# Kernel tuning notes

Hardware: AMD Instinct MI355X
Metric: run time of the kernel (lower is better)

Reference implementation:

```python
import jax, jax.numpy as jnp
import numpy as np

HID = 64
EPS = 1e-12  # tf.contrib.layers.layer_norm variance_epsilon


def _ln(x, g, b):
    m = jnp.mean(x, axis=-1, keepdims=True)
    v = jnp.mean(jnp.square(x - m), axis=-1, keepdims=True)
    return (x - m) * jax.lax.rsqrt(v + EPS) * g + b


def setup_inputs() -> dict:
    key = jax.random.key(0)
    k1, k2, k3, k4 = jax.random.split(key, 4)
    N, T, OBS, ACT = 2048, 256, 96, 32
    D = OBS + ACT
    obss = jax.random.normal(k1, (N, T, OBS), dtype=jnp.float32)
    actions = jax.random.normal(k2, (N, T, ACT), dtype=jnp.float32)
    W = jax.random.normal(k3, (D + HID, 4 * HID), dtype=jnp.float32) * (1.0 / np.sqrt(D + HID))
    ln_gamma = jnp.ones((5, HID), dtype=jnp.float32)   # i, j, f, o, state norms
    ln_beta = jnp.zeros((5, HID), dtype=jnp.float32)
    dense_W = jax.random.uniform(k4, (HID, 1), dtype=jnp.float32, minval=-0.003, maxval=0.003)
    dense_b = jnp.zeros((1,), dtype=jnp.float32)
    return {"obss": obss, "actions": actions, "W": W, "ln_gamma": ln_gamma,
            "ln_beta": ln_beta, "dense_W": dense_W, "dense_b": dense_b}


def reference(obss, actions, W, ln_gamma, ln_beta, dense_W, dense_b):
    # [N,T,obs+act] -> time-major [T,N,D]
    x = jnp.concatenate([obss, actions], axis=-1)
    xt = jnp.transpose(x, (1, 0, 2))
    N = x.shape[0]
    c0 = jnp.zeros((N, HID), dtype=x.dtype)
    h0 = jnp.zeros((N, HID), dtype=x.dtype)
    forget_bias = jnp.asarray(1.0, dtype=x.dtype)

    def step(carry, x_t):
        c, h = carry
        z = jnp.concatenate([x_t, h], axis=-1) @ W  # [N, 4*HID], no bias
        i, j, f, o = jnp.split(z, 4, axis=-1)
        i = _ln(i, ln_gamma[0], ln_beta[0])
        j = _ln(j, ln_gamma[1], ln_beta[1])
        f = _ln(f, ln_gamma[2], ln_beta[2])
        o = _ln(o, ln_gamma[3], ln_beta[3])
        new_c = c * jax.nn.sigmoid(f + forget_bias) + jax.nn.sigmoid(i) * jnp.tanh(j)
        new_c = _ln(new_c, ln_gamma[4], ln_beta[4])
        new_h = jnp.tanh(new_c) * jax.nn.sigmoid(o)
        return (new_c, new_h), new_h

    _, hs = jax.lax.scan(step, (c0, h0), xt)  # hs: [T,N,HID]
    outputs = jnp.transpose(hs, (1, 0, 2))     # [N,T,HID]
    q = outputs @ dense_W + dense_b            # [N,T,1]
    return q
```

## Files before the change

### kernel.cpp

```cpp
#include <hip/hip_runtime.h>

#define TT 256
#define OBS 96
#define ACTD 32
#define RPB 8
#define CH 8
#define XCS 136
#define ZXS 12
#define ZBS 69
#define HBS 80
#define EPS 1e-12f

typedef _Float16 f16x8 __attribute__((ext_vector_type(8)));
typedef float f32x4 __attribute__((ext_vector_type(4)));
typedef unsigned short u16x8 __attribute__((ext_vector_type(8)));
typedef unsigned int u32;
typedef unsigned short u16;

__device__ __forceinline__ u16 f2h(float f) {
  return __builtin_bit_cast(u16, (_Float16)f);
}
__device__ __forceinline__ u32 pk2h(float a, float b) {
  return (u32)f2h(a) | ((u32)f2h(b) << 16);
}
__device__ __forceinline__ float sigm(float x) { return 1.0f / (1.0f + __expf(-x)); }
__device__ __forceinline__ float tanh_(float x) { return 1.0f - 2.0f / (__expf(2.0f * x) + 1.0f); }

template <int CTRL>
__device__ __forceinline__ float dpp_add(float x) {
  int t = __builtin_amdgcn_update_dpp(0, __builtin_bit_cast(int, x), CTRL, 0xF, 0xF, true);
  return x + __builtin_bit_cast(float, t);
}
__device__ __forceinline__ float red16(float x) {
  x = dpp_add<0xB1>(x);
  x = dpp_add<0x4E>(x);
  x = dpp_add<0x124>(x);
  x = dpp_add<0x128>(x);
  return x;
}
__device__ __forceinline__ float red64(float x) {
  x = red16(x);
  x += __shfl_xor(x, 16, 64);
  x += __shfl_xor(x, 32, 64);
  return x;
}

__device__ __forceinline__ void barrier_lds() {
  __builtin_amdgcn_sched_barrier(0);
  asm volatile("s_waitcnt lgkmcnt(0)" ::: "memory");
  __builtin_amdgcn_s_barrier();
  __builtin_amdgcn_sched_barrier(0);
}

__global__ __launch_bounds__(512, 2) void lstm_fused(
    const float* __restrict__ obss, const float* __restrict__ actions,
    const float* __restrict__ Wm, const float* __restrict__ gamma,
    const float* __restrict__ beta, const float* __restrict__ dWv,
    const float* __restrict__ dbv, float* __restrict__ out)
{
  __shared__ u16 xchunk[CH][RPB][XCS];
  __shared__ float zxT[CH][256][ZXS];
  __shared__ float zbuf[4][16][ZBS];
  __shared__ float pbuf[4][16][4];
  __shared__ u16 hh[CH][RPB][HBS];

  const int tid = threadIdx.x;
  const int wv = tid >> 6;
  const int ln = tid & 63;
  const int l15 = ln & 15;
  const int quad = ln >> 4;
  const int g = wv & 3;
  const int half = wv >> 2;
  const int n0 = blockIdx.x * RPB;
  const int c0 = g * 64 + half * 32 + l15;

  for (int i = tid; i < CH * RPB * HBS / 2; i += 512) ((u32*)hh)[i] = 0u;

  u16x8 bw[6][2];
  #pragma unroll
  for (int kt = 0; kt < 6; ++kt)
    #pragma unroll
    for (int nt = 0; nt < 2; ++nt)
      #pragma unroll
      for (int j = 0; j < 8; ++j)
        bw[kt][nt][j] = f2h(Wm[(kt * 32 + quad * 8 + j) * 256 + c0 + nt * 16]);

  float ggam[4], gbet[4];
  #pragma unroll
  for (int gg = 0; gg < 4; ++gg) {
    ggam[gg] = gamma[gg * 64 + ln];
    gbet[gg] = beta[gg * 64 + ln];
  }
  const float cgam = gamma[4 * 64 + ln], cbet = beta[4 * 64 + ln];
  const float dw = dWv[ln];
  const float bias = dbv[0];

  const int sp = tid >> 8;
  const int srow = (tid >> 5) & 7;
  const int slot = tid & 31;
  const float* obs_p = obss + (size_t)(n0 + srow) * TT * OBS;
  const float* act_p = actions + (size_t)(n0 + srow) * TT * ACTD;

  f32x4 xst[4];
  #pragma unroll
  for (int k = 0; k < 4; ++k) {
    const int s = sp + 2 * k;
    xst[k] = (slot < 24) ? *(const f32x4*)(obs_p + s * OBS + slot * 4)
                         : *(const f32x4*)(act_p + s * ACTD + (slot - 24) * 4);
  }
  #pragma unroll
  for (int k = 0; k < 4; ++k) {
    const int s = sp + 2 * k;
    *(uint2*)&xchunk[s][srow][slot * 4] =
        make_uint2(pk2h(xst[k][0], xst[k][1]), pk2h(xst[k][2], xst[k][3]));
  }

  float creg = 0.0f;
  f32x4 zs0p, zs1p;
  __syncthreads();

  for (int t = 0; t < TT; ++t) {
    const int tm = t & 7;
    const int tp = (t + 7) & 7;

    if (tm == 0) {
      if (t > 0) {
        #pragma unroll
        for (int s = 0; s < CH; ++s) {
          const float hv = (float)__builtin_bit_cast(_Float16, hh[s][wv][ln]);
          const float qv = red64(hv * dw);
          if (ln == 0) out[(size_t)(n0 + wv) * TT + (t - 8) + s] = qv + bias;
        }
      }
      #pragma unroll
      for (int k = 0; k < 4; ++k) {
        int tl = t + 8 + sp + 2 * k; if (tl > TT - 1) tl = TT - 1;
        xst[k] = (slot < 24) ? *(const f32x4*)(obs_p + tl * OBS + slot * 4)
                             : *(const f32x4*)(act_p + tl * ACTD + (slot - 24) * 4);
      }
      #pragma unroll
      for (int s = 0; s < CH; ++s) {
        u16x8 afx[4];
        #pragma unroll
        for (int kt = 0; kt < 4; ++kt)
          afx[kt] = *(const u16x8*)&xchunk[s][l15 & 7][kt * 32 + quad * 8];
        f32x4 ax0 = {0.f, 0.f, 0.f, 0.f}, ax1 = ax0;
        #pragma unroll
        for (int kt = 0; kt < 4; ++kt) {
          ax0 = __builtin_amdgcn_mfma_f32_16x16x32_f16(
              __builtin_bit_cast(f16x8, afx[kt]), __builtin_bit_cast(f16x8, bw[kt][0]), ax0, 0, 0, 0);
          ax1 = __builtin_amdgcn_mfma_f32_16x16x32_f16(
              __builtin_bit_cast(f16x8, afx[kt]), __builtin_bit_cast(f16x8, bw[kt][1]), ax1, 0, 0, 0);
        }
        if (quad < 2) {
          *(f32x4*)&zxT[s][c0][quad * 4] = ax0;
          *(f32x4*)&zxT[s][c0 + 16][quad * 4] = ax1;
        }
      }
    }

    const u16x8 afh0 = *(const u16x8*)&hh[tp][l15 & 7][quad * 8];
    const u16x8 afh1 = *(const u16x8*)&hh[tp][l15 & 7][32 + quad * 8];
    const f32x4 zs0 = (tm == 0) ? *(const f32x4*)&zxT[0][c0][(quad & 1) * 4] : zs0p;
    const f32x4 zs1 = (tm == 0) ? *(const f32x4*)&zxT[0][c0 + 16][(quad & 1) * 4] : zs1p;
    f32x4 acc0 = __builtin_amdgcn_mfma_f32_16x16x32_f16(
        __builtin_bit_cast(f16x8, afh0), __builtin_bit_cast(f16x8, bw[4][0]), zs0, 0, 0, 0);
    f32x4 acc1 = __builtin_amdgcn_mfma_f32_16x16x32_f16(
        __builtin_bit_cast(f16x8, afh0), __builtin_bit_cast(f16x8, bw[4][1]), zs1, 0, 0, 0);
    acc0 = __builtin_amdgcn_mfma_f32_16x16x32_f16(
        __builtin_bit_cast(f16x8, afh1), __builtin_bit_cast(f16x8, bw[5][0]), acc0, 0, 0, 0);
    acc1 = __builtin_amdgcn_mfma_f32_16x16x32_f16(
        __builtin_bit_cast(f16x8, afh1), __builtin_bit_cast(f16x8, bw[5][1]), acc1, 0, 0, 0);

    #pragma unroll
    for (int r = 0; r < 4; ++r) {
      zbuf[g][quad * 4 + r][half * 32 + l15]      = acc0[r];
      zbuf[g][quad * 4 + r][half * 32 + 16 + l15] = acc1[r];
    }
    float s[4], ss[4];
    #pragma unroll
    for (int r = 0; r < 4; ++r) {
      s[r]  = red16(acc0[r] + acc1[r]);
      ss[r] = red16(acc0[r] * acc0[r] + acc1[r] * acc1[r]);
    }
    if (l15 < 4) {
      const float sv  = l15 == 0 ? s[0]  : l15 == 1 ? s[1]  : l15 == 2 ? s[2]  : s[3];
      const float ssv = l15 == 0 ? ss[0] : l15 == 1 ? ss[1] : l15 == 2 ? ss[2] : ss[3];
      *(float2*)&pbuf[g][quad * 4 + l15][half * 2] = make_float2(sv, ssv);
    }
    barrier_lds();

    if (tm != 7) {
      zs0p = *(const f32x4*)&zxT[tm + 1][c0][(quad & 1) * 4];
      zs1p = *(const f32x4*)&zxT[tm + 1][c0 + 16][(quad & 1) * 4];
    }
    float zc[4];
    #pragma unroll
    for (int gg = 0; gg < 4; ++gg) {
      const f32x4 p = *(const f32x4*)&pbuf[gg][wv][0];
      const float mean = (p[0] + p[2]) * (1.0f / 64.0f);
      const float var  = (p[1] + p[3]) * (1.0f / 64.0f) - mean * mean;
      const float rstd = rsqrtf(var + EPS);
      zc[gg] = (zbuf[gg][wv][ln] - mean) * rstd * ggam[gg] + gbet[gg];
    }
    const float nc = creg * sigm(zc[2] + 1.0f) + sigm(zc[0]) * tanh_(zc[1]);
    const float s2  = red64(nc);
    const float ss2 = red64(nc * nc);
    const float mean = s2 * (1.0f / 64.0f);
    const float var  = ss2 * (1.0f / 64.0f) - mean * mean;
    const float rstd = rsqrtf(var + EPS);
    const float cn = (nc - mean) * rstd * cgam + cbet;
    creg = cn;
    const float h = tanh_(cn) * sigm(zc[3]);
    hh[tm][wv][ln] = f2h(h);

    if (tm == 7) {
      #pragma unroll
      for (int k = 0; k < 4; ++k) {
        const int scm = sp + 2 * k;
        *(uint2*)&xchunk[scm][srow][slot * 4] =
            make_uint2(pk2h(xst[k][0], xst[k][1]), pk2h(xst[k][2], xst[k][3]));
      }
    }
    barrier_lds();
  }

  #pragma unroll
  for (int s = 0; s < CH; ++s) {
    const float hv = (float)__builtin_bit_cast(_Float16, hh[s][wv][ln]);
    const float qv = red64(hv * dw);
    if (ln == 0) out[(size_t)(n0 + wv) * TT + 248 + s] = qv + bias;
  }
}

extern "C" void kernel_launch(void* const* d_in, const int* in_sizes, int n_in,
                              void* d_out, int out_size, void* d_ws, size_t ws_size,
                              hipStream_t stream) {
  const float* obss    = (const float*)d_in[0];
  const float* actions = (const float*)d_in[1];
  const float* Wm      = (const float*)d_in[2];
  const float* gamma   = (const float*)d_in[3];
  const float* beta    = (const float*)d_in[4];
  const float* dWv     = (const float*)d_in[5];
  const float* dbv     = (const float*)d_in[6];
  float* out = (float*)d_out;
  lstm_fused<<<dim3(2048 / RPB), dim3(512), 0, stream>>>(obss, actions, Wm, gamma,
                                                         beta, dWv, dbv, out);
}
```

Measured before the change: 689.8 us.

## Warp-specialize LSTM kernel: consumer waves run recurrence, producer waves precompute input projection

Splits the 8 waves into 4 consumer waves that do the recurrent h@W matmul, layer norms and cell update for two rows each, and 4 producer waves. The producers compute the next chunk's input projection into a double-buffered fp16 zxT, prefetch x tiles and emit the dense outputs, all spread across timesteps. The intent is to take the periodic input-projection burst and the output reduction off the serial recurrence path. In exchange, zxT is stored as fp16 (lower precision), the producers reload W from global memory each chunk, and consumer waves now do twice the per-row elementwise work.

```diff
diff --git a/kernel.cpp b/kernel.cpp
--- a/kernel.cpp
+++ b/kernel.cpp
@@ -8,7 +8,7 @@
 #define XCS 136
 #define ZXS 12
 #define ZBS 69
-#define HBS 80
+#define HBS 72
 #define EPS 1e-12f
 
 typedef _Float16 f16x8 __attribute__((ext_vector_type(8)));
@@ -22,6 +22,12 @@
 }
 __device__ __forceinline__ u32 pk2h(float a, float b) {
   return (u32)f2h(a) | ((u32)f2h(b) << 16);
+}
+__device__ __forceinline__ float h2f_lo(u32 v) {
+  return (float)__builtin_bit_cast(_Float16, (u16)(v & 0xffffu));
+}
+__device__ __forceinline__ float h2f_hi(u32 v) {
+  return (float)__builtin_bit_cast(_Float16, (u16)(v >> 16));
 }
 __device__ __forceinline__ float sigm(float x) { return 1.0f / (1.0f + __expf(-x)); }
 __device__ __forceinline__ float tanh_(float x) { return 1.0f - 2.0f / (__expf(2.0f * x) + 1.0f); }
@@ -58,11 +64,11 @@
     const float* __restrict__ beta, const float* __restrict__ dWv,
     const float* __restrict__ dbv, float* __restrict__ out)
 {
-  __shared__ u16 xchunk[CH][RPB][XCS];
-  __shared__ float zxT[CH][256][ZXS];
-  __shared__ float zbuf[4][16][ZBS];
-  __shared__ float pbuf[4][16][4];
-  __shared__ u16 hh[CH][RPB][HBS];
+  __shared__ u16 xchunk[2][CH][RPB][XCS];
+  __shared__ u16 zxT[2][CH][256][ZXS];
+  __shared__ float zbuf[4][RPB][ZBS];
+  __shared__ float pbuf[4][RPB][2];
+  __shared__ u16 hh[2][CH][RPB][HBS];
 
   const int tid = threadIdx.x;
   const int wv = tid >> 6;
@@ -70,166 +76,214 @@
   const int l15 = ln & 15;
   const int quad = ln >> 4;
   const int g = wv & 3;
-  const int half = wv >> 2;
+  const bool cons = wv < 4;
   const int n0 = blockIdx.x * RPB;
-  const int c0 = g * 64 + half * 32 + l15;
-
-  for (int i = tid; i < CH * RPB * HBS / 2; i += 512) ((u32*)hh)[i] = 0u;
-
-  u16x8 bw[6][2];
-  #pragma unroll
-  for (int kt = 0; kt < 6; ++kt)
-    #pragma unroll
-    for (int nt = 0; nt < 2; ++nt)
-      #pragma unroll
-      for (int j = 0; j < 8; ++j)
-        bw[kt][nt][j] = f2h(Wm[(kt * 32 + quad * 8 + j) * 256 + c0 + nt * 16]);
-
-  float ggam[4], gbet[4];
-  #pragma unroll
-  for (int gg = 0; gg < 4; ++gg) {
-    ggam[gg] = gamma[gg * 64 + ln];
-    gbet[gg] = beta[gg * 64 + ln];
-  }
-  const float cgam = gamma[4 * 64 + ln], cbet = beta[4 * 64 + ln];
-  const float dw = dWv[ln];
-  const float bias = dbv[0];
-
-  const int sp = tid >> 8;
+
+  for (int i = tid; i < 2 * CH * RPB * HBS / 2; i += 512) ((u32*)hh)[i] = 0u;
+
+  const int oct01 = tid >> 8;
   const int srow = (tid >> 5) & 7;
   const int slot = tid & 31;
   const float* obs_p = obss + (size_t)(n0 + srow) * TT * OBS;
   const float* act_p = actions + (size_t)(n0 + srow) * TT * ACTD;
 
-  f32x4 xst[4];
   #pragma unroll
-  for (int k = 0; k < 4; ++k) {
-    const int s = sp + 2 * k;
-    xst[k] = (slot < 24) ? *(const f32x4*)(obs_p + s * OBS + slot * 4)
-                         : *(const f32x4*)(act_p + s * ACTD + (slot - 24) * 4);
-  }
-  #pragma unroll
-  for (int k = 0; k < 4; ++k) {
-    const int s = sp + 2 * k;
-    *(uint2*)&xchunk[s][srow][slot * 4] =
-        make_uint2(pk2h(xst[k][0], xst[k][1]), pk2h(xst[k][2], xst[k][3]));
-  }
-
-  float creg = 0.0f;
-  f32x4 zs0p, zs1p;
+  for (int s = 0; s < CH; ++s) {
+    const int tl = oct01 * 8 + s;
+    const f32x4 v = (slot < 24) ? *(const f32x4*)(obs_p + tl * OBS + slot * 4)
+                                : *(const f32x4*)(act_p + tl * ACTD + (slot - 24) * 4);
+    *(uint2*)&xchunk[oct01][s][srow][slot * 4] =
+        make_uint2(pk2h(v[0], v[1]), pk2h(v[2], v[3]));
+  }
+
+  u16x8 bwh[2][4];
+  float ggam[4], gbet[4];
+  float cgam = 0.f, cbet = 0.f;
+  if (cons) {
+    #pragma unroll
+    for (int kt = 0; kt < 2; ++kt)
+      #pragma unroll
+      for (int ct = 0; ct < 4; ++ct)
+        #pragma unroll
+        for (int j = 0; j < 8; ++j)
+          bwh[kt][ct][j] =
+              f2h(Wm[(128 + kt * 32 + quad * 8 + j) * 256 + g * 64 + ct * 16 + l15]);
+    #pragma unroll
+    for (int gg = 0; gg < 4; ++gg) {
+      ggam[gg] = gamma[gg * 64 + ln];
+      gbet[gg] = beta[gg * 64 + ln];
+    }
+    cgam = gamma[4 * 64 + ln]; cbet = beta[4 * 64 + ln];
+  }
+  const float dw = dWv[ln];
+  const float bias = dbv[0];
+
   __syncthreads();
+
+  if (!cons) {
+    #pragma unroll
+    for (int ct = 0; ct < 4; ++ct) {
+      const int col = g * 64 + ct * 16 + l15;
+      u16x8 fr[4];
+      #pragma unroll
+      for (int kt = 0; kt < 4; ++kt)
+        #pragma unroll
+        for (int j = 0; j < 8; ++j)
+          fr[kt][j] = f2h(Wm[(kt * 32 + quad * 8 + j) * 256 + col]);
+      #pragma unroll
+      for (int s = 0; s < CH; ++s) {
+        f32x4 ax = {0.f, 0.f, 0.f, 0.f};
+        #pragma unroll
+        for (int kt = 0; kt < 4; ++kt) {
+          const u16x8 afx = *(const u16x8*)&xchunk[0][s][l15 & 7][kt * 32 + quad * 8];
+          ax = __builtin_amdgcn_mfma_f32_16x16x32_f16(
+              __builtin_bit_cast(f16x8, afx), __builtin_bit_cast(f16x8, fr[kt]), ax, 0, 0, 0);
+        }
+        if (quad < 2)
+          *(uint2*)&zxT[0][s][col][quad * 4] =
+              make_uint2(pk2h(ax[0], ax[1]), pk2h(ax[2], ax[3]));
+      }
+    }
+  }
+  __syncthreads();
+
+  float creg0 = 0.f, creg1 = 0.f;
 
   for (int t = 0; t < TT; ++t) {
     const int tm = t & 7;
-    const int tp = (t + 7) & 7;
-
-    if (tm == 0) {
-      if (t > 0) {
+    const int o = t >> 3;
+    const int buf = o & 1, nb = buf ^ 1;
+
+    if (cons) {
+      const int rb = (tm == 0) ? nb : buf;
+      const int tp = (tm == 0) ? 7 : tm - 1;
+      const u16x8 afh0 = *(const u16x8*)&hh[rb][tp][l15 & 7][quad * 8];
+      const u16x8 afh1 = *(const u16x8*)&hh[rb][tp][l15 & 7][32 + quad * 8];
+      f32x4 acc[4];
+      #pragma unroll
+      for (int ct = 0; ct < 4; ++ct) {
+        f32x4 a = {0.f, 0.f, 0.f, 0.f};
+        a = __builtin_amdgcn_mfma_f32_16x16x32_f16(
+            __builtin_bit_cast(f16x8, afh0), __builtin_bit_cast(f16x8, bwh[0][ct]), a, 0, 0, 0);
+        a = __builtin_amdgcn_mfma_f32_16x16x32_f16(
+            __builtin_bit_cast(f16x8, afh1), __builtin_bit_cast(f16x8, bwh[1][ct]), a, 0, 0, 0);
+        const uint2 zx = *(const uint2*)&zxT[buf][tm][g * 64 + ct * 16 + l15][(quad & 1) * 4];
+        a[0] += h2f_lo(zx.x); a[1] += h2f_hi(zx.x);
+        a[2] += h2f_lo(zx.y); a[3] += h2f_hi(zx.y);
+        acc[ct] = a;
+      }
+      if (quad < 2) {
+        #pragma unroll
+        for (int ct = 0; ct < 4; ++ct)
+          #pragma unroll
+          for (int r = 0; r < 4; ++r)
+            zbuf[g][quad * 4 + r][ct * 16 + l15] = acc[ct][r];
+      }
+      float s[4], ss[4];
+      #pragma unroll
+      for (int r = 0; r < 4; ++r) {
+        s[r]  = red16((acc[0][r] + acc[1][r]) + (acc[2][r] + acc[3][r]));
+        ss[r] = red16((acc[0][r] * acc[0][r] + acc[1][r] * acc[1][r]) +
+                      (acc[2][r] * acc[2][r] + acc[3][r] * acc[3][r]));
+      }
+      if (quad < 2 && l15 < 4) {
+        const float sv  = l15 == 0 ? s[0]  : l15 == 1 ? s[1]  : l15 == 2 ? s[2]  : s[3];
+        const float ssv = l15 == 0 ? ss[0] : l15 == 1 ? ss[1] : l15 == 2 ? ss[2] : ss[3];
+        *(float2*)&pbuf[g][quad * 4 + l15][0] = make_float2(sv, ssv);
+      }
+    } else {
+      if (tm < 4 && t < TT - 8) {
+        const int ct = tm;
+        const int col = g * 64 + ct * 16 + l15;
+        u16x8 fr[4];
+        #pragma unroll
+        for (int kt = 0; kt < 4; ++kt)
+          #pragma unroll
+          for (int j = 0; j < 8; ++j)
+            fr[kt][j] = f2h(Wm[(kt * 32 + quad * 8 + j) * 256 + col]);
         #pragma unroll
         for (int s = 0; s < CH; ++s) {
-          const float hv = (float)__builtin_bit_cast(_Float16, hh[s][wv][ln]);
-          const float qv = red64(hv * dw);
-          if (ln == 0) out[(size_t)(n0 + wv) * TT + (t - 8) + s] = qv + bias;
+          f32x4 ax = {0.f, 0.f, 0.f, 0.f};
+          #pragma unroll
+          for (int kt = 0; kt < 4; ++kt) {
+            const u16x8 afx = *(const u16x8*)&xchunk[nb][s][l15 & 7][kt * 32 + quad * 8];
+            ax = __builtin_amdgcn_mfma_f32_16x16x32_f16(
+                __builtin_bit_cast(f16x8, afx), __builtin_bit_cast(f16x8, fr[kt]), ax, 0, 0, 0);
+          }
+          if (quad < 2)
+            *(uint2*)&zxT[nb][s][col][quad * 4] =
+                make_uint2(pk2h(ax[0], ax[1]), pk2h(ax[2], ax[3]));
         }
       }
-      #pragma unroll
-      for (int k = 0; k < 4; ++k) {
-        int tl = t + 8 + sp + 2 * k; if (tl > TT - 1) tl = TT - 1;
-        xst[k] = (slot < 24) ? *(const f32x4*)(obs_p + tl * OBS + slot * 4)
-                             : *(const f32x4*)(act_p + tl * ACTD + (slot - 24) * 4);
-      }
-      #pragma unroll
-      for (int s = 0; s < CH; ++s) {
-        u16x8 afx[4];
-        #pragma unroll
-        for (int kt = 0; kt < 4; ++kt)
-          afx[kt] = *(const u16x8*)&xchunk[s][l15 & 7][kt * 32 + quad * 8];
-        f32x4 ax0 = {0.f, 0.f, 0.f, 0.f}, ax1 = ax0;
-        #pragma unroll
-        for (int kt = 0; kt < 4; ++kt) {
-          ax0 = __builtin_amdgcn_mfma_f32_16x16x32_f16(
-              __builtin_bit_cast(f16x8, afx[kt]), __builtin_bit_cast(f16x8, bw[kt][0]), ax0, 0, 0, 0);
-          ax1 = __builtin_amdgcn_mfma_f32_16x16x32_f16(
-              __builtin_bit_cast(f16x8, afx[kt]), __builtin_bit_cast(f16x8, bw[kt][1]), ax1, 0, 0, 0);
+      if (t >= 8) {
+        const int ra = 2 * (wv - 4);
+        const float hv0 = (float)__builtin_bit_cast(_Float16, hh[nb][tm][ra][ln]);
+        const float hv1 = (float)__builtin_bit_cast(_Float16, hh[nb][tm][ra + 1][ln]);
+        const float q0 = red64(hv0 * dw);
+        const float q1 = red64(hv1 * dw);
+        if (ln == 0) {
+          out[(size_t)(n0 + ra) * TT + (t - 8)] = q0 + bias;
+          out[(size_t)(n0 + ra + 1) * TT + (t - 8)] = q1 + bias;
         }
-        if (quad < 2) {
-          *(f32x4*)&zxT[s][c0][quad * 4] = ax0;
-          *(f32x4*)&zxT[s][c0 + 16][quad * 4] = ax1;
+      }
+    }
+    barrier_lds();
+
+    if (cons) {
+      float zc0[4], zc1[4];
+      #pragma unroll
+      for (int gg = 0; gg < 4; ++gg) {
+        const float2 pa = *(const float2*)&pbuf[gg][g][0];
+        const float2 pb = *(const float2*)&pbuf[gg][g + 4][0];
+        const float m0 = pa.x * (1.0f / 64.0f);
+        const float v0 = pa.y * (1.0f / 64.0f) - m0 * m0;
+        const float m1 = pb.x * (1.0f / 64.0f);
+        const float v1 = pb.y * (1.0f / 64.0f) - m1 * m1;
+        zc0[gg] = (zbuf[gg][g][ln] - m0) * rsqrtf(v0 + EPS) * ggam[gg] + gbet[gg];
+        zc1[gg] = (zbuf[gg][g + 4][ln] - m1) * rsqrtf(v1 + EPS) * ggam[gg] + gbet[gg];
+      }
+      const float nc0 = creg0 * sigm(zc0[2] + 1.0f) + sigm(zc0[0]) * tanh_(zc0[1]);
+      const float nc1 = creg1 * sigm(zc1[2] + 1.0f) + sigm(zc1[0]) * tanh_(zc1[1]);
+      const float s20 = red64(nc0), ss20 = red64(nc0 * nc0);
+      const float s21 = red64(nc1), ss21 = red64(nc1 * nc1);
+      const float mm0 = s20 * (1.0f / 64.0f), vv0 = ss20 * (1.0f / 64.0f) - mm0 * mm0;
+      const float mm1 = s21 * (1.0f / 64.0f), vv1 = ss21 * (1.0f / 64.0f) - mm1 * mm1;
+      const float cn0 = (nc0 - mm0) * rsqrtf(vv0 + EPS) * cgam + cbet;
+      const float cn1 = (nc1 - mm1) * rsqrtf(vv1 + EPS) * cgam + cbet;
+      creg0 = cn0; creg1 = cn1;
+      const float h0 = tanh_(cn0) * sigm(zc0[3]);
+      const float h1 = tanh_(cn1) * sigm(zc1[3]);
+      hh[buf][tm][g][ln] = f2h(h0);
+      hh[buf][tm][g + 4][ln] = f2h(h1);
+    } else {
+      if (tm >= 4 && o < 30) {
+        #pragma unroll
+        for (int k = 0; k < 2; ++k) {
+          const int s = (tm - 4) * 2 + k;
+          const int tl = (o + 2) * 8 + s;
+          const f32x4 v = (slot < 24) ? *(const f32x4*)(obs_p + tl * OBS + slot * 4)
+                                      : *(const f32x4*)(act_p + tl * ACTD + (slot - 24) * 4);
+          *(uint2*)&xchunk[buf][s][srow][slot * 4] =
+              make_uint2(pk2h(v[0], v[1]), pk2h(v[2], v[3]));
         }
       }
     }
-
-    const u16x8 afh0 = *(const u16x8*)&hh[tp][l15 & 7][quad * 8];
-    const u16x8 afh1 = *(const u16x8*)&hh[tp][l15 & 7][32 + quad * 8];
-    const f32x4 zs0 = (tm == 0) ? *(const f32x4*)&zxT[0][c0][(quad & 1) * 4] : zs0p;
-    const f32x4 zs1 = (tm == 0) ? *(const f32x4*)&zxT[0][c0 + 16][(quad & 1) * 4] : zs1p;
-    f32x4 acc0 = __builtin_amdgcn_mfma_f32_16x16x32_f16(
-        __builtin_bit_cast(f16x8, afh0), __builtin_bit_cast(f16x8, bw[4][0]), zs0, 0, 0, 0);
-    f32x4 acc1 = __builtin_amdgcn_mfma_f32_16x16x32_f16(
-        __builtin_bit_cast(f16x8, afh0), __builtin_bit_cast(f16x8, bw[4][1]), zs1, 0, 0, 0);
-    acc0 = __builtin_amdgcn_mfma_f32_16x16x32_f16(
-        __builtin_bit_cast(f16x8, afh1), __builtin_bit_cast(f16x8, bw[5][0]), acc0, 0, 0, 0);
-    acc1 = __builtin_amdgcn_mfma_f32_16x16x32_f16(
-        __builtin_bit_cast(f16x8, afh1), __builtin_bit_cast(f16x8, bw[5][1]), acc1, 0, 0, 0);
-
+    barrier_lds();
+  }
+
+  if (!cons) {
+    const int ra = 2 * (wv - 4);
     #pragma unroll
-    for (int r = 0; r < 4; ++r) {
-      zbuf[g][quad * 4 + r][half * 32 + l15]      = acc0[r];
-      zbuf[g][quad * 4 + r][half * 32 + 16 + l15] = acc1[r];
-    }
-    float s[4], ss[4];
-    #pragma unroll
-    for (int r = 0; r < 4; ++r) {
-      s[r]  = red16(acc0[r] + acc1[r]);
-      ss[r] = red16(acc0[r] * acc0[r] + acc1[r] * acc1[r]);
-    }
-    if (l15 < 4) {
-      const float sv  = l15 == 0 ? s[0]  : l15 == 1 ? s[1]  : l15 == 2 ? s[2]  : s[3];
-      const float ssv = l15 == 0 ? ss[0] : l15 == 1 ? ss[1] : l15 == 2 ? ss[2] : ss[3];
-      *(float2*)&pbuf[g][quad * 4 + l15][half * 2] = make_float2(sv, ssv);
-    }
-    barrier_lds();
-
-    if (tm != 7) {
-      zs0p = *(const f32x4*)&zxT[tm + 1][c0][(quad & 1) * 4];
-      zs1p = *(const f32x4*)&zxT[tm + 1][c0 + 16][(quad & 1) * 4];
-    }
-    float zc[4];
-    #pragma unroll
-    for (int gg = 0; gg < 4; ++gg) {
-      const f32x4 p = *(const f32x4*)&pbuf[gg][wv][0];
-      const float mean = (p[0] + p[2]) * (1.0f / 64.0f);
-      const float var  = (p[1] + p[3]) * (1.0f / 64.0f) - mean * mean;
-      const float rstd = rsqrtf(var + EPS);
-      zc[gg] = (zbuf[gg][wv][ln] - mean) * rstd * ggam[gg] + gbet[gg];
-    }
-    const float nc = creg * sigm(zc[2] + 1.0f) + sigm(zc[0]) * tanh_(zc[1]);
-    const float s2  = red64(nc);
-    const float ss2 = red64(nc * nc);
-    const float mean = s2 * (1.0f / 64.0f);
-    const float var  = ss2 * (1.0f / 64.0f) - mean * mean;
-    const float rstd = rsqrtf(var + EPS);
-    const float cn = (nc - mean) * rstd * cgam + cbet;
-    creg = cn;
-    const float h = tanh_(cn) * sigm(zc[3]);
-    hh[tm][wv][ln] = f2h(h);
-
-    if (tm == 7) {
-      #pragma unroll
-      for (int k = 0; k < 4; ++k) {
-        const int scm = sp + 2 * k;
-        *(uint2*)&xchunk[scm][srow][slot * 4] =
-            make_uint2(pk2h(xst[k][0], xst[k][1]), pk2h(xst[k][2], xst[k][3]));
-      }
-    }
-    barrier_lds();
-  }
-
-  #pragma unroll
-  for (int s = 0; s < CH; ++s) {
-    const float hv = (float)__builtin_bit_cast(_Float16, hh[s][wv][ln]);
-    const float qv = red64(hv * dw);
-    if (ln == 0) out[(size_t)(n0 + wv) * TT + 248 + s] = qv + bias;
+    for (int s = 0; s < CH; ++s) {
+      const float hv0 = (float)__builtin_bit_cast(_Float16, hh[1][s][ra][ln]);
+      const float hv1 = (float)__builtin_bit_cast(_Float16, hh[1][s][ra + 1][ln]);
+      const float q0 = red64(hv0 * dw);
+      const float q1 = red64(hv1 * dw);
+      if (ln == 0) {
+        out[(size_t)(n0 + ra) * TT + 248 + s] = q0 + bias;
+        out[(size_t)(n0 + ra + 1) * TT + 248 + s] = q1 + bias;
+      }
+    }
   }
 }
 
```

Measured after the change: 819.9 us. 1.19x slower.
